# Optimization experiments

Measured on AMD Instinct MI355X. Metric: run time of the kernel, lower is better.

The kernel has to match this reference:

```python
import jax, jax.numpy as jnp
import numpy as np

B, I, H, L, D, O = 2048, 512, 512, 32, 1024, 512
TEMP = 1.0


def _make_params(key):
    ks = jax.random.split(key, 16)
    s = 0.05
    p = {}
    p['in_W'] = jax.random.normal(ks[0], (H, I), jnp.float32) * s
    p['in_b'] = jnp.zeros((H,), jnp.float32)
    p['out_W'] = jax.random.normal(ks[1], (O, H), jnp.float32) * s
    p['out_b'] = jnp.zeros((O,), jnp.float32)
    p['enc_Wih'] = jax.random.normal(ks[2], (4 * H, H), jnp.float32) * s
    p['enc_Whh'] = jax.random.normal(ks[3], (4 * H, H), jnp.float32) * s
    p['enc_bih'] = jnp.zeros((4 * H,), jnp.float32)
    p['enc_bhh'] = jnp.zeros((4 * H,), jnp.float32)
    p['dec_Wih'] = jax.random.normal(ks[4], (4 * H, H), jnp.float32) * s
    p['dec_Whh'] = jax.random.normal(ks[5], (4 * H, H), jnp.float32) * s
    p['dec_bih'] = jnp.zeros((4 * H,), jnp.float32)
    p['dec_bhh'] = jnp.zeros((4 * H,), jnp.float32)
    p['h2t_W'] = jax.random.normal(ks[6], (D, H), jnp.float32) * s
    p['h2t_b'] = jnp.zeros((D,), jnp.float32)
    p['t2h_W'] = jax.random.normal(ks[7], (H, D), jnp.float32) * s
    p['t2h_b'] = jnp.zeros((H,), jnp.float32)
    return p


def setup_inputs() -> dict:
    key = jax.random.key(0)
    k1, k2, k3 = jax.random.split(key, 3)
    inp = {'x': jax.random.normal(k1, (B, I), jnp.float32),
           'gumbel': jax.random.gumbel(k2, (L, B, D), jnp.float32)}
    inp.update(_make_params(k3))
    return inp


def _lstm_cell(x, h, c, Wih, Whh, bih, bhh):
    gates = x @ Wih.T + bih + h @ Whh.T + bhh  # [B, 4H]
    i, f, g, o = jnp.split(gates, 4, axis=-1)
    i = jax.nn.sigmoid(i); f = jax.nn.sigmoid(f)
    g = jnp.tanh(g); o = jax.nn.sigmoid(o)
    c_new = f * c + i * g
    h_new = o * jnp.tanh(c_new)
    return h_new, c_new


def reference(x, gumbel, in_W, in_b, out_W, out_b,
              enc_Wih, enc_Whh, enc_bih, enc_bhh,
              dec_Wih, dec_Whh, dec_bih, dec_bhh,
              h2t_W, h2t_b, t2h_W, t2h_b):
    # ---- encode ----
    x_emb = x @ in_W.T + in_b                      # [B, H]
    hx0 = jnp.zeros((B, H), x.dtype)
    inp0 = jnp.zeros((B, H), x.dtype)

    def enc_step(carry, g_noise):
        hx, cx, inp = carry
        hx, cx = _lstm_cell(inp, hx, cx, enc_Wih, enc_Whh, enc_bih, enc_bhh)
        pre = hx @ h2t_W.T + h2t_b                 # [B, D]
        soft = jax.nn.softmax((pre + g_noise) / TEMP, axis=-1)
        amax = jnp.argmax(soft, axis=-1)           # [B]
        oh = jax.nn.one_hot(amax, D, dtype=soft.dtype)
        z = soft + jax.lax.stop_gradient(oh - soft)  # straight-through
        inp = z @ t2h_W.T + t2h_b
        return (hx, cx, inp), (z, pre, amax)

    # initial cell state is the embedded input (cx = x), per the source
    _, (z_seq, logit_seq, msg_seq) = jax.lax.scan(
        enc_step, (hx0, x_emb, inp0), gumbel)
    one_hot = jnp.transpose(z_seq, (1, 0, 2))      # [B, L, D]
    logits = jnp.transpose(logit_seq, (1, 0, 2))   # [B, L, D]
    messages = msg_seq.T                           # [B, L]

    # ---- decode ----
    z_emb = z_seq @ t2h_W.T + t2h_b                # [L, B, H]

    def dec_step(carry, inp):
        hx, cx = carry
        hx, cx = _lstm_cell(inp, hx, cx, dec_Wih, dec_Whh, dec_bih, dec_bhh)
        return (hx, cx), None

    (hx_final, _), _ = jax.lax.scan(
        dec_step, (jnp.zeros((B, H), x.dtype), jnp.zeros((B, H), x.dtype)), z_emb)
    recon = hx_final @ out_W.T + out_b             # [B, O]
    return recon, one_hot, logits, messages
```

## Files before the change

kernel.cpp:

```cpp
#include <hip/hip_runtime.h>
#include <math.h>

#define B_  2048
#define I_  512
#define H_  512
#define L_  32
#define D_  1024
#define O_  512
#define H4_ 2048
#define KC  32

typedef _Float16 f16x8 __attribute__((ext_vector_type(8)));
typedef _Float16 f16x4 __attribute__((ext_vector_type(4)));
typedef float    f32x4 __attribute__((ext_vector_type(4)));

#define SPLIT_S  1024.0f
#define SPLIT_RS 0.0009765625f

__device__ __forceinline__ void gload16(const _Float16* g, _Float16* l) {
    __builtin_amdgcn_global_load_lds(
        (const __attribute__((address_space(1))) void*)g,
        (__attribute__((address_space(3))) void*)l, 16, 0, 0);
}

__device__ __forceinline__ f16x8 lds_frag(const _Float16* base, int row, int ko) {
    int off = row * 64 + ((((ko >> 3) ^ (row & 7))) << 3);
    return *(const f16x8*)(base + off);
}

__global__ __launch_bounds__(256) void gemm_atb(
    const float* __restrict__ A, const float* __restrict__ W,
    const float* __restrict__ bias, float* __restrict__ C, int ldc,
    float* __restrict__ C2, int ldc2,
    int M, int N, int K)
{
    __shared__ __align__(16) float As[KC][68];
    __shared__ __align__(16) float Ws[KC][68];
    const int tx = threadIdx.x & 15, ty = threadIdx.x >> 4;
    const int m0 = blockIdx.y * 64, n0 = blockIdx.x * 64;
    float acc[4][4] = {};

    for (int k0 = 0; k0 < K; k0 += KC) {
#pragma unroll
        for (int p = 0; p < 2; ++p) {
            int q = threadIdx.x + 256 * p;
            int r = q >> 3, c = q & 7;
            float4 va = *reinterpret_cast<const float4*>(
                &A[(long long)(m0 + r) * K + k0 + c * 4]);
            As[c * 4 + 0][r] = va.x; As[c * 4 + 1][r] = va.y;
            As[c * 4 + 2][r] = va.z; As[c * 4 + 3][r] = va.w;
            float4 vw = *reinterpret_cast<const float4*>(
                &W[(long long)(n0 + r) * K + k0 + c * 4]);
            Ws[c * 4 + 0][r] = vw.x; Ws[c * 4 + 1][r] = vw.y;
            Ws[c * 4 + 2][r] = vw.z; Ws[c * 4 + 3][r] = vw.w;
        }
        __syncthreads();
#pragma unroll
        for (int kk = 0; kk < KC; ++kk) {
            float4 a = *reinterpret_cast<const float4*>(&As[kk][ty * 4]);
            float4 w = *reinterpret_cast<const float4*>(&Ws[kk][tx * 4]);
            float av[4] = {a.x, a.y, a.z, a.w};
            float wv[4] = {w.x, w.y, w.z, w.w};
#pragma unroll
            for (int i = 0; i < 4; ++i)
#pragma unroll
                for (int j = 0; j < 4; ++j)
                    acc[i][j] = fmaf(av[i], wv[j], acc[i][j]);
        }
        __syncthreads();
    }

#pragma unroll
    for (int i = 0; i < 4; ++i) {
        int m = m0 + ty * 4 + i;
        int n = n0 + tx * 4;
        float4 out;
        out.x = acc[i][0]; out.y = acc[i][1]; out.z = acc[i][2]; out.w = acc[i][3];
        if (bias) {
            out.x += bias[n + 0]; out.y += bias[n + 1];
            out.z += bias[n + 2]; out.w += bias[n + 3];
        }
        *reinterpret_cast<float4*>(&C[(long long)m * ldc + n]) = out;
        if (C2)
            *reinterpret_cast<float4*>(&C2[(long long)m * ldc2 + n]) = out;
    }
}

__global__ __launch_bounds__(256) void split_f16(
    const float* __restrict__ src, _Float16* __restrict__ d1,
    _Float16* __restrict__ d2, int n4)
{
    int i = blockIdx.x * 256 + threadIdx.x;
    if (i >= n4) return;
    float4 v = reinterpret_cast<const float4*>(src)[i];
    float vv[4] = {v.x, v.y, v.z, v.w};
    f16x4 o1, o2;
#pragma unroll
    for (int j = 0; j < 4; ++j) {
        _Float16 hh = (_Float16)vv[j];
        o1[j] = hh;
        o2[j] = (_Float16)((vv[j] - (float)hh) * SPLIT_S);
    }
    *reinterpret_cast<f16x4*>(d1 + 4 * i) = o1;
    *reinterpret_cast<f16x4*>(d2 + 4 * i) = o2;
}

__global__ __launch_bounds__(512) void lstm_step_mfma(
    const _Float16* __restrict__ hx1, const _Float16* __restrict__ hx2,
    float* __restrict__ cx,
    const _Float16* __restrict__ W1, const _Float16* __restrict__ W2,
    const float* __restrict__ P,
    const int* __restrict__ m_prev,
    const float* __restrict__ bih, const float* __restrict__ bhh,
    _Float16* __restrict__ ho1, _Float16* __restrict__ ho2,
    float* __restrict__ hof)
{
    __shared__ __align__(16) _Float16 As1[128 * 64];
    __shared__ __align__(16) _Float16 As2[128 * 64];
    __shared__ __align__(16) _Float16 Ws1[128 * 64];
    __shared__ __align__(16) _Float16 Ws2[128 * 64];
    __shared__ int ms[128];

    const int tid = threadIdx.x;
    const int m0 = blockIdx.y * 128, h0 = blockIdx.x * 32;
    const int l = tid & 63, wid = tid >> 6;
    const int wm = wid >> 1, wn = wid & 1;

    if (m_prev != nullptr && tid < 128) ms[tid] = m_prev[m0 + tid];

    f32x4 accM[2][4] = {};
    f32x4 accC[2][4] = {};

    for (int k0 = 0; k0 < H_; k0 += 64) {
#pragma unroll
        for (int s = 0; s < 2; ++s) {
            int seg = wid + s * 8;
            int r   = seg * 8 + (l >> 3);
            int jsw = ((l & 7) ^ (l >> 3)) << 3;
            size_t ga = (size_t)(m0 + r) * H_ + k0 + jsw;
            gload16(hx1 + ga, &As1[seg * 512]);
            gload16(hx2 + ga, &As2[seg * 512]);
            int wrow = ((r >> 4) & 3) * H_ + h0 + ((r >> 6) << 4) + (r & 15);
            size_t gw = (size_t)wrow * H_ + k0 + jsw;
            gload16(W1 + gw, &Ws1[seg * 512]);
            gload16(W2 + gw, &Ws2[seg * 512]);
        }
        __syncthreads();
        const int ac = (l >> 4) << 3;
        const int arow = wm * 32 + (l & 15);
        const int brow = wn * 64 + (l & 15);
#pragma unroll
        for (int kc = 0; kc < 2; ++kc) {
            int ko = kc * 32 + ac;
            f16x8 b1[4], b2[4];
#pragma unroll
            for (int fn = 0; fn < 4; ++fn) {
                b1[fn] = lds_frag(Ws1, brow + fn * 16, ko);
                b2[fn] = lds_frag(Ws2, brow + fn * 16, ko);
            }
#pragma unroll
            for (int fm = 0; fm < 2; ++fm) {
                f16x8 a1 = lds_frag(As1, arow + fm * 16, ko);
                f16x8 a2 = lds_frag(As2, arow + fm * 16, ko);
#pragma unroll
                for (int fn = 0; fn < 4; ++fn) {
                    accM[fm][fn] = __builtin_amdgcn_mfma_f32_16x16x32_f16(
                        a1, b1[fn], accM[fm][fn], 0, 0, 0);
                    accC[fm][fn] = __builtin_amdgcn_mfma_f32_16x16x32_f16(
                        a1, b2[fn], accC[fm][fn], 0, 0, 0);
                    accC[fm][fn] = __builtin_amdgcn_mfma_f32_16x16x32_f16(
                        a2, b1[fn], accC[fm][fn], 0, 0, 0);
                }
            }
        }
        __syncthreads();
    }

    const int hl = l & 15;
    const int h  = h0 + wn * 16 + hl;
    const int rb = m0 + wm * 32 + ((l >> 4) << 2);
    float bs0 = bih[0 * H_ + h] + bhh[0 * H_ + h];
    float bs1 = bih[1 * H_ + h] + bhh[1 * H_ + h];
    float bs2 = bih[2 * H_ + h] + bhh[2 * H_ + h];
    float bs3 = bih[3 * H_ + h] + bhh[3 * H_ + h];
#pragma unroll
    for (int fm = 0; fm < 2; ++fm) {
#pragma unroll
        for (int rg = 0; rg < 4; ++rg) {
            int b = rb + fm * 16 + rg;
            float g0 = accM[fm][0][rg] + SPLIT_RS * accC[fm][0][rg] + bs0;
            float g1 = accM[fm][1][rg] + SPLIT_RS * accC[fm][1][rg] + bs1;
            float g2 = accM[fm][2][rg] + SPLIT_RS * accC[fm][2][rg] + bs2;
            float g3 = accM[fm][3][rg] + SPLIT_RS * accC[fm][3][rg] + bs3;
            if (m_prev != nullptr) {
                const float* Pr = P + (size_t)ms[b - m0] * H4_;
                g0 += Pr[0 * H_ + h]; g1 += Pr[1 * H_ + h];
                g2 += Pr[2 * H_ + h]; g3 += Pr[3 * H_ + h];
            }
            float ig = 1.f / (1.f + expf(-g0));
            float fg = 1.f / (1.f + expf(-g1));
            float gg = tanhf(g2);
            float og = 1.f / (1.f + expf(-g3));
            size_t off = (size_t)b * H_ + h;
            float cnew = fg * cx[off] + ig * gg;
            cx[off] = cnew;
            float hv = og * tanhf(cnew);
            _Float16 hh1 = (_Float16)hv;
            ho1[off] = hh1;
            ho2[off] = (_Float16)((hv - (float)hh1) * SPLIT_S);
            if (hof != nullptr) hof[off] = hv;
        }
    }
}

__global__ __launch_bounds__(256) void gemm_pre_fused(
    const _Float16* __restrict__ A1, const _Float16* __restrict__ A2,
    const _Float16* __restrict__ W1, const _Float16* __restrict__ W2,
    const float* __restrict__ bias,
    float* __restrict__ C2, int ldc2,
    const float* __restrict__ gum,
    float* __restrict__ pbest, int* __restrict__ pidx)
{
    __shared__ __align__(16) _Float16 As1[64 * 64];
    __shared__ __align__(16) _Float16 As2[64 * 64];
    __shared__ __align__(16) _Float16 Ws1[128 * 64];
    __shared__ __align__(16) _Float16 Ws2[128 * 64];
    __shared__ float cb[2][64];
    __shared__ int   ci[2][64];

    const int tid = threadIdx.x;
    const int m0 = blockIdx.y * 64, n0 = blockIdx.x * 128;
    const int l = tid & 63, wid = tid >> 6;
    const int wm = wid >> 1, wn = wid & 1;

    f32x4 accM[2][4] = {};
    f32x4 accC[2][4] = {};

    for (int k0 = 0; k0 < H_; k0 += 64) {
#pragma unroll
        for (int s = 0; s < 2; ++s) {
            int seg = wid + s * 4;
            int r   = seg * 8 + (l >> 3);
            int jsw = ((l & 7) ^ (l >> 3)) << 3;
            size_t ga = (size_t)(m0 + r) * H_ + k0 + jsw;
            gload16(A1 + ga, &As1[seg * 512]);
            gload16(A2 + ga, &As2[seg * 512]);
        }
#pragma unroll
        for (int s = 0; s < 4; ++s) {
            int seg = wid + s * 4;
            int r   = seg * 8 + (l >> 3);
            int jsw = ((l & 7) ^ (l >> 3)) << 3;
            size_t gw = (size_t)(n0 + r) * H_ + k0 + jsw;
            gload16(W1 + gw, &Ws1[seg * 512]);
            gload16(W2 + gw, &Ws2[seg * 512]);
        }
        __syncthreads();
        const int ac = (l >> 4) << 3;
        const int arow = wm * 32 + (l & 15);
        const int brow = wn * 64 + (l & 15);
#pragma unroll
        for (int kc = 0; kc < 2; ++kc) {
            int ko = kc * 32 + ac;
            f16x8 b1[4], b2[4];
#pragma unroll
            for (int fn = 0; fn < 4; ++fn) {
                b1[fn] = lds_frag(Ws1, brow + fn * 16, ko);
                b2[fn] = lds_frag(Ws2, brow + fn * 16, ko);
            }
#pragma unroll
            for (int fm = 0; fm < 2; ++fm) {
                f16x8 a1 = lds_frag(As1, arow + fm * 16, ko);
                f16x8 a2 = lds_frag(As2, arow + fm * 16, ko);
#pragma unroll
                for (int fn = 0; fn < 4; ++fn) {
                    accM[fm][fn] = __builtin_amdgcn_mfma_f32_16x16x32_f16(
                        a1, b1[fn], accM[fm][fn], 0, 0, 0);
                    accC[fm][fn] = __builtin_amdgcn_mfma_f32_16x16x32_f16(
                        a1, b2[fn], accC[fm][fn], 0, 0, 0);
                    accC[fm][fn] = __builtin_amdgcn_mfma_f32_16x16x32_f16(
                        a2, b1[fn], accC[fm][fn], 0, 0, 0);
                }
            }
        }
        __syncthreads();
    }

    const int hl = l & 15;
    const int g4 = l >> 4;
    const int rb = m0 + wm * 32 + (g4 << 2);
    float vbest[2][4]; int vidx[2][4];
#pragma unroll
    for (int fm = 0; fm < 2; ++fm)
#pragma unroll
        for (int rg = 0; rg < 4; ++rg) { vbest[fm][rg] = -INFINITY; vidx[fm][rg] = 0; }

#pragma unroll
    for (int fn = 0; fn < 4; ++fn) {
        int d = n0 + wn * 64 + fn * 16 + hl;
        float bv = bias[d];
#pragma unroll
        for (int fm = 0; fm < 2; ++fm)
#pragma unroll
            for (int rg = 0; rg < 4; ++rg) {
                int b = rb + fm * 16 + rg;
                float v = accM[fm][fn][rg] + SPLIT_RS * accC[fm][fn][rg] + bv;
                C2[(size_t)b * ldc2 + d] = v;
                float t = v + gum[(size_t)b * D_ + d];
                if (t > vbest[fm][rg]) { vbest[fm][rg] = t; vidx[fm][rg] = d; }
            }
    }

#pragma unroll
    for (int off = 1; off < 16; off <<= 1) {
#pragma unroll
        for (int fm = 0; fm < 2; ++fm)
#pragma unroll
            for (int rg = 0; rg < 4; ++rg) {
                float ov = __shfl_xor(vbest[fm][rg], off);
                int   oi = __shfl_xor(vidx[fm][rg], off);
                if (ov > vbest[fm][rg] ||
                    (ov == vbest[fm][rg] && oi < vidx[fm][rg])) {
                    vbest[fm][rg] = ov; vidx[fm][rg] = oi;
                }
            }
    }
    if (hl == 0) {
#pragma unroll
        for (int fm = 0; fm < 2; ++fm)
#pragma unroll
            for (int rg = 0; rg < 4; ++rg) {
                int rl = wm * 32 + fm * 16 + (g4 << 2) + rg;
                cb[wn][rl] = vbest[fm][rg];
                ci[wn][rl] = vidx[fm][rg];
            }
    }
    __syncthreads();
    if (tid < 64) {
        float b0 = cb[0][tid]; int i0 = ci[0][tid];
        float b1v = cb[1][tid]; int i1 = ci[1][tid];
        if (b1v > b0 || (b1v == b0 && i1 < i0)) { b0 = b1v; i0 = i1; }
        pbest[(size_t)(m0 + tid) * 8 + blockIdx.x] = b0;
        pidx [(size_t)(m0 + tid) * 8 + blockIdx.x] = i0;
    }
}

__global__ __launch_bounds__(256) void argmax_fin(
    const float* __restrict__ pbest, const int* __restrict__ pidx,
    float* __restrict__ onehot, float* __restrict__ messages,
    int* __restrict__ m_out, int l)
{
    int b = blockIdx.x * 256 + threadIdx.x;
    float best = -INFINITY; int bi = 0;
#pragma unroll
    for (int j = 0; j < 8; ++j) {
        float v = pbest[(size_t)b * 8 + j];
        int   i = pidx [(size_t)b * 8 + j];
        if (v > best || (v == best && i < bi)) { best = v; bi = i; }
    }
    m_out[b] = bi;
    messages[(size_t)b * L_ + l] = (float)bi;
    onehot[((size_t)b * L_ + l) * D_ + bi] = 1.0f;
}

__global__ __launch_bounds__(256) void build_emb(
    const float* __restrict__ t2h_W, const float* __restrict__ t2h_b,
    float* __restrict__ emb)
{
    int idx = blockIdx.x * 256 + threadIdx.x;
    int d = idx >> 9, h = idx & (H_ - 1);
    emb[idx] = t2h_W[(long long)h * D_ + d] + t2h_b[h];
}

extern "C" void kernel_launch(void* const* d_in, const int* in_sizes, int n_in,
                              void* d_out, int out_size, void* d_ws, size_t ws_size,
                              hipStream_t stream)
{
    (void)in_sizes; (void)n_in; (void)out_size; (void)ws_size;
    const float* x       = (const float*)d_in[0];
    const float* gumbel  = (const float*)d_in[1];
    const float* in_W    = (const float*)d_in[2];
    const float* in_b    = (const float*)d_in[3];
    const float* out_W   = (const float*)d_in[4];
    const float* out_b   = (const float*)d_in[5];
    const float* enc_Wih = (const float*)d_in[6];
    const float* enc_Whh = (const float*)d_in[7];
    const float* enc_bih = (const float*)d_in[8];
    const float* enc_bhh = (const float*)d_in[9];
    const float* dec_Wih = (const float*)d_in[10];
    const float* dec_Whh = (const float*)d_in[11];
    const float* dec_bih = (const float*)d_in[12];
    const float* dec_bhh = (const float*)d_in[13];
    const float* h2t_W   = (const float*)d_in[14];
    const float* h2t_b   = (const float*)d_in[15];
    const float* t2h_W   = (const float*)d_in[16];
    const float* t2h_b   = (const float*)d_in[17];

    float* out      = (float*)d_out;
    float* recon    = out;
    float* onehot   = out + (size_t)B_ * O_;
    float* logits   = onehot + (size_t)B_ * L_ * D_;
    float* messages = logits + (size_t)B_ * L_ * D_;

    float* ws    = (float*)d_ws;
    float* cx    = ws;
    float* emb   = cx + (size_t)B_ * H_;
    float* P_enc = emb + (size_t)D_ * H_;
    float* P_dec = P_enc + (size_t)D_ * H4_;
    float* hxf   = P_dec + (size_t)D_ * H4_;
    float* pbest = hxf + (size_t)B_ * H_;
    int*   pidx  = (int*)(pbest + (size_t)B_ * 8);
    int*   m_all = pidx + (size_t)B_ * 8;
    _Float16* fb   = (_Float16*)(m_all + (size_t)L_ * B_);
    _Float16* hxA1 = fb;  fb += (size_t)B_ * H_;
    _Float16* hxA2 = fb;  fb += (size_t)B_ * H_;
    _Float16* hxB1 = fb;  fb += (size_t)B_ * H_;
    _Float16* hxB2 = fb;  fb += (size_t)B_ * H_;
    _Float16* encW1 = fb; fb += (size_t)H4_ * H_;
    _Float16* encW2 = fb; fb += (size_t)H4_ * H_;
    _Float16* decW1 = fb; fb += (size_t)H4_ * H_;
    _Float16* decW2 = fb; fb += (size_t)H4_ * H_;
    _Float16* h2t1  = fb; fb += (size_t)D_ * H_;
    _Float16* h2t2  = fb;

    const dim3 blk256(256);

    hipMemsetAsync(hxA1, 0, (size_t)B_ * H_ * 4, stream);
    hipMemsetAsync(onehot, 0, (size_t)B_ * L_ * D_ * sizeof(float), stream);

    split_f16<<<dim3((H4_ * H_ / 4) / 256), blk256, 0, stream>>>(
        enc_Whh, encW1, encW2, H4_ * H_ / 4);
    split_f16<<<dim3((H4_ * H_ / 4) / 256), blk256, 0, stream>>>(
        dec_Whh, decW1, decW2, H4_ * H_ / 4);
    split_f16<<<dim3((D_ * H_ / 4) / 256), blk256, 0, stream>>>(
        h2t_W, h2t1, h2t2, D_ * H_ / 4);

    gemm_atb<<<dim3(H_ / 64, B_ / 64), blk256, 0, stream>>>(
        x, in_W, in_b, cx, H_, nullptr, 0, B_, H_, I_);

    build_emb<<<dim3((D_ * H_) / 256), blk256, 0, stream>>>(t2h_W, t2h_b, emb);
    gemm_atb<<<dim3(H4_ / 64, D_ / 64), blk256, 0, stream>>>(
        emb, enc_Wih, nullptr, P_enc, H4_, nullptr, 0, D_, H4_, H_);
    gemm_atb<<<dim3(H4_ / 64, D_ / 64), blk256, 0, stream>>>(
        emb, dec_Wih, nullptr, P_dec, H4_, nullptr, 0, D_, H4_, H_);

    _Float16 *c1 = hxA1, *c2 = hxA2, *n1 = hxB1, *n2 = hxB2;
    for (int l = 0; l < L_; ++l) {
        lstm_step_mfma<<<dim3(H_ / 32, B_ / 128), dim3(512), 0, stream>>>(
            c1, c2, cx, encW1, encW2, P_enc,
            (l == 0) ? nullptr : (m_all + (size_t)(l - 1) * B_),
            enc_bih, enc_bhh, n1, n2, nullptr);
        { _Float16* t = c1; c1 = n1; n1 = t; t = c2; c2 = n2; n2 = t; }
        gemm_pre_fused<<<dim3(D_ / 128, B_ / 64), blk256, 0, stream>>>(
            c1, c2, h2t1, h2t2, h2t_b,
            logits + (size_t)l * D_, L_ * D_,
            gumbel + (size_t)l * B_ * D_, pbest, pidx);
        argmax_fin<<<dim3(B_ / 256), blk256, 0, stream>>>(
            pbest, pidx, onehot, messages, m_all + (size_t)l * B_, l);
    }

    hipMemsetAsync(c1, 0, (size_t)B_ * H_ * 2, stream);
    hipMemsetAsync(c2, 0, (size_t)B_ * H_ * 2, stream);
    hipMemsetAsync(cx, 0, (size_t)B_ * H_ * sizeof(float), stream);
    for (int l = 0; l < L_; ++l) {
        lstm_step_mfma<<<dim3(H_ / 32, B_ / 128), dim3(512), 0, stream>>>(
            c1, c2, cx, decW1, decW2, P_dec, m_all + (size_t)l * B_,
            dec_bih, dec_bhh, n1, n2, (l == L_ - 1) ? hxf : nullptr);
        { _Float16* t = c1; c1 = n1; n1 = t; t = c2; c2 = n2; n2 = t; }
    }

    gemm_atb<<<dim3(O_ / 64, B_ / 64), blk256, 0, stream>>>(
        hxf, out_W, out_b, recon, O_, nullptr, 0, B_, O_, H_);
}
```

Before: 3.169 ms.

## Double-buffer LDS tiles in LSTM and logits GEMMs and fuse argmax finalize

Both the LSTM step kernel and the fused logits GEMM now keep two LDS buffers, so the async global-to-LDS loads for the next K tile are issued while MFMAs run on the current one. The separate argmax_fin launch per encoder step is removed. Instead the last block to finish each row group, found with an atomic counter and threadfences, reduces the partial maxima and writes the message and one-hot entry. This doubles LDS use, which may lower occupancy, and adds atomic/fence overhead in exchange for fewer launches and overlapped loads.

Result: slower. 3.555 ms (+12.2%).

```diff
diff --git a/kernel.cpp b/kernel.cpp
--- a/kernel.cpp
+++ b/kernel.cpp
@@ -115,15 +115,15 @@
     _Float16* __restrict__ ho1, _Float16* __restrict__ ho2,
     float* __restrict__ hof)
 {
-    __shared__ __align__(16) _Float16 As1[128 * 64];
-    __shared__ __align__(16) _Float16 As2[128 * 64];
-    __shared__ __align__(16) _Float16 Ws1[128 * 64];
-    __shared__ __align__(16) _Float16 Ws2[128 * 64];
+    __shared__ __align__(16) _Float16 As1[2][128 * 64];
+    __shared__ __align__(16) _Float16 As2[2][128 * 64];
+    __shared__ __align__(16) _Float16 Ws1[2][128 * 64];
+    __shared__ __align__(16) _Float16 Ws2[2][128 * 64];
     __shared__ int ms[128];
 
     const int tid = threadIdx.x;
     const int m0 = blockIdx.y * 128, h0 = blockIdx.x * 32;
-    const int l = tid & 63, wid = tid >> 6;
+    const int ln = tid & 63, wid = tid >> 6;
     const int wm = wid >> 1, wn = wid & 1;
 
     if (m_prev != nullptr && tid < 128) ms[tid] = m_prev[m0 + tid];
@@ -131,37 +131,49 @@
     f32x4 accM[2][4] = {};
     f32x4 accC[2][4] = {};
 
-    for (int k0 = 0; k0 < H_; k0 += 64) {
+    auto stage = [&](int buf, int k0) {
 #pragma unroll
         for (int s = 0; s < 2; ++s) {
             int seg = wid + s * 8;
-            int r   = seg * 8 + (l >> 3);
-            int jsw = ((l & 7) ^ (l >> 3)) << 3;
+            int r   = seg * 8 + (ln >> 3);
+            int jsw = ((ln & 7) ^ (ln >> 3)) << 3;
             size_t ga = (size_t)(m0 + r) * H_ + k0 + jsw;
-            gload16(hx1 + ga, &As1[seg * 512]);
-            gload16(hx2 + ga, &As2[seg * 512]);
+            gload16(hx1 + ga, &As1[buf][seg * 512]);
+            gload16(hx2 + ga, &As2[buf][seg * 512]);
             int wrow = ((r >> 4) & 3) * H_ + h0 + ((r >> 6) << 4) + (r & 15);
             size_t gw = (size_t)wrow * H_ + k0 + jsw;
-            gload16(W1 + gw, &Ws1[seg * 512]);
-            gload16(W2 + gw, &Ws2[seg * 512]);
-        }
-        __syncthreads();
-        const int ac = (l >> 4) << 3;
-        const int arow = wm * 32 + (l & 15);
-        const int brow = wn * 64 + (l & 15);
+            gload16(W1 + gw, &Ws1[buf][seg * 512]);
+            gload16(W2 + gw, &Ws2[buf][seg * 512]);
+        }
+    };
+
+    stage(0, 0);
+    __syncthreads();
+
+    const int ac = (ln >> 4) << 3;
+    const int arow = wm * 32 + (ln & 15);
+    const int brow = wn * 64 + (ln & 15);
+    int cur = 0;
+
+    for (int t = 0; t < 8; ++t) {
+        if (t < 7) stage(cur ^ 1, (t + 1) * 64);
+        const _Float16* a1b = &As1[cur][0];
+        const _Float16* a2b = &As2[cur][0];
+        const _Float16* w1b = &Ws1[cur][0];
+        const _Float16* w2b = &Ws2[cur][0];
 #pragma unroll
         for (int kc = 0; kc < 2; ++kc) {
             int ko = kc * 32 + ac;
             f16x8 b1[4], b2[4];
 #pragma unroll
             for (int fn = 0; fn < 4; ++fn) {
-                b1[fn] = lds_frag(Ws1, brow + fn * 16, ko);
-                b2[fn] = lds_frag(Ws2, brow + fn * 16, ko);
+                b1[fn] = lds_frag(w1b, brow + fn * 16, ko);
+                b2[fn] = lds_frag(w2b, brow + fn * 16, ko);
             }
 #pragma unroll
             for (int fm = 0; fm < 2; ++fm) {
-                f16x8 a1 = lds_frag(As1, arow + fm * 16, ko);
-                f16x8 a2 = lds_frag(As2, arow + fm * 16, ko);
+                f16x8 a1 = lds_frag(a1b, arow + fm * 16, ko);
+                f16x8 a2 = lds_frag(a2b, arow + fm * 16, ko);
 #pragma unroll
                 for (int fn = 0; fn < 4; ++fn) {
                     accM[fm][fn] = __builtin_amdgcn_mfma_f32_16x16x32_f16(
@@ -174,11 +186,12 @@
             }
         }
         __syncthreads();
-    }
-
-    const int hl = l & 15;
+        cur ^= 1;
+    }
+
+    const int hl = ln & 15;
     const int h  = h0 + wn * 16 + hl;
-    const int rb = m0 + wm * 32 + ((l >> 4) << 2);
+    const int rb = m0 + wm * 32 + ((ln >> 4) << 2);
     float bs0 = bih[0 * H_ + h] + bhh[0 * H_ + h];
     float bs1 = bih[1 * H_ + h] + bhh[1 * H_ + h];
     float bs2 = bih[2 * H_ + h] + bhh[2 * H_ + h];
@@ -219,59 +232,75 @@
     const float* __restrict__ bias,
     float* __restrict__ C2, int ldc2,
     const float* __restrict__ gum,
-    float* __restrict__ pbest, int* __restrict__ pidx)
+    float* __restrict__ pbest, int* __restrict__ pidx,
+    int* __restrict__ cnt,
+    float* __restrict__ onehot, float* __restrict__ messages,
+    int* __restrict__ m_out, int l)
 {
-    __shared__ __align__(16) _Float16 As1[64 * 64];
-    __shared__ __align__(16) _Float16 As2[64 * 64];
-    __shared__ __align__(16) _Float16 Ws1[128 * 64];
-    __shared__ __align__(16) _Float16 Ws2[128 * 64];
+    __shared__ __align__(16) _Float16 As1[2][64 * 64];
+    __shared__ __align__(16) _Float16 As2[2][64 * 64];
+    __shared__ __align__(16) _Float16 Ws1[2][128 * 64];
+    __shared__ __align__(16) _Float16 Ws2[2][128 * 64];
     __shared__ float cb[2][64];
     __shared__ int   ci[2][64];
+    __shared__ int   lastf;
 
     const int tid = threadIdx.x;
     const int m0 = blockIdx.y * 64, n0 = blockIdx.x * 128;
-    const int l = tid & 63, wid = tid >> 6;
+    const int ln = tid & 63, wid = tid >> 6;
     const int wm = wid >> 1, wn = wid & 1;
 
     f32x4 accM[2][4] = {};
     f32x4 accC[2][4] = {};
 
-    for (int k0 = 0; k0 < H_; k0 += 64) {
+    auto stage = [&](int buf, int k0) {
 #pragma unroll
         for (int s = 0; s < 2; ++s) {
             int seg = wid + s * 4;
-            int r   = seg * 8 + (l >> 3);
-            int jsw = ((l & 7) ^ (l >> 3)) << 3;
+            int r   = seg * 8 + (ln >> 3);
+            int jsw = ((ln & 7) ^ (ln >> 3)) << 3;
             size_t ga = (size_t)(m0 + r) * H_ + k0 + jsw;
-            gload16(A1 + ga, &As1[seg * 512]);
-            gload16(A2 + ga, &As2[seg * 512]);
+            gload16(A1 + ga, &As1[buf][seg * 512]);
+            gload16(A2 + ga, &As2[buf][seg * 512]);
         }
 #pragma unroll
         for (int s = 0; s < 4; ++s) {
             int seg = wid + s * 4;
-            int r   = seg * 8 + (l >> 3);
-            int jsw = ((l & 7) ^ (l >> 3)) << 3;
+            int r   = seg * 8 + (ln >> 3);
+            int jsw = ((ln & 7) ^ (ln >> 3)) << 3;
             size_t gw = (size_t)(n0 + r) * H_ + k0 + jsw;
-            gload16(W1 + gw, &Ws1[seg * 512]);
-            gload16(W2 + gw, &Ws2[seg * 512]);
-        }
-        __syncthreads();
-        const int ac = (l >> 4) << 3;
-        const int arow = wm * 32 + (l & 15);
-        const int brow = wn * 64 + (l & 15);
+            gload16(W1 + gw, &Ws1[buf][seg * 512]);
+            gload16(W2 + gw, &Ws2[buf][seg * 512]);
+        }
+    };
+
+    stage(0, 0);
+    __syncthreads();
+
+    const int ac = (ln >> 4) << 3;
+    const int arow = wm * 32 + (ln & 15);
+    const int brow = wn * 64 + (ln & 15);
+    int cur = 0;
+
+    for (int t = 0; t < 8; ++t) {
+        if (t < 7) stage(cur ^ 1, (t + 1) * 64);
+        const _Float16* a1b = &As1[cur][0];
+        const _Float16* a2b = &As2[cur][0];
+        const _Float16* w1b = &Ws1[cur][0];
+        const _Float16* w2b = &Ws2[cur][0];
 #pragma unroll
         for (int kc = 0; kc < 2; ++kc) {
             int ko = kc * 32 + ac;
             f16x8 b1[4], b2[4];
 #pragma unroll
             for (int fn = 0; fn < 4; ++fn) {
-                b1[fn] = lds_frag(Ws1, brow + fn * 16, ko);
-                b2[fn] = lds_frag(Ws2, brow + fn * 16, ko);
+                b1[fn] = lds_frag(w1b, brow + fn * 16, ko);
+                b2[fn] = lds_frag(w2b, brow + fn * 16, ko);
             }
 #pragma unroll
             for (int fm = 0; fm < 2; ++fm) {
-                f16x8 a1 = lds_frag(As1, arow + fm * 16, ko);
-                f16x8 a2 = lds_frag(As2, arow + fm * 16, ko);
+                f16x8 a1 = lds_frag(a1b, arow + fm * 16, ko);
+                f16x8 a2 = lds_frag(a2b, arow + fm * 16, ko);
 #pragma unroll
                 for (int fn = 0; fn < 4; ++fn) {
                     accM[fm][fn] = __builtin_amdgcn_mfma_f32_16x16x32_f16(
@@ -284,10 +313,11 @@
             }
         }
         __syncthreads();
-    }
-
-    const int hl = l & 15;
-    const int g4 = l >> 4;
+        cur ^= 1;
+    }
+
+    const int hl = ln & 15;
+    const int g4 = ln >> 4;
     const int rb = m0 + wm * 32 + (g4 << 2);
     float vbest[2][4]; int vidx[2][4];
 #pragma unroll
@@ -342,25 +372,29 @@
         if (b1v > b0 || (b1v == b0 && i1 < i0)) { b0 = b1v; i0 = i1; }
         pbest[(size_t)(m0 + tid) * 8 + blockIdx.x] = b0;
         pidx [(size_t)(m0 + tid) * 8 + blockIdx.x] = i0;
-    }
-}
-
-__global__ __launch_bounds__(256) void argmax_fin(
-    const float* __restrict__ pbest, const int* __restrict__ pidx,
-    float* __restrict__ onehot, float* __restrict__ messages,
-    int* __restrict__ m_out, int l)
-{
-    int b = blockIdx.x * 256 + threadIdx.x;
-    float best = -INFINITY; int bi = 0;
-#pragma unroll
-    for (int j = 0; j < 8; ++j) {
-        float v = pbest[(size_t)b * 8 + j];
-        int   i = pidx [(size_t)b * 8 + j];
-        if (v > best || (v == best && i < bi)) { best = v; bi = i; }
-    }
-    m_out[b] = bi;
-    messages[(size_t)b * L_ + l] = (float)bi;
-    onehot[((size_t)b * L_ + l) * D_ + bi] = 1.0f;
+        __threadfence();
+    }
+    __syncthreads();
+    if (tid == 0)
+        lastf = (atomicAdd(cnt + blockIdx.y, 1) == 7);
+    __syncthreads();
+    if (lastf) {
+        __threadfence();
+        if (tid < 64) {
+            int b = m0 + tid;
+            volatile const float* pb = pbest + (size_t)b * 8;
+            volatile const int*   pi = pidx  + (size_t)b * 8;
+            float best = -INFINITY; int bi = 0;
+#pragma unroll
+            for (int j = 0; j < 8; ++j) {
+                float v = pb[j]; int i = pi[j];
+                if (v > best || (v == best && i < bi)) { best = v; bi = i; }
+            }
+            m_out[b] = bi;
+            messages[(size_t)b * L_ + l] = (float)bi;
+            onehot[((size_t)b * L_ + l) * D_ + bi] = 1.0f;
+        }
+    }
 }
 
 __global__ __launch_bounds__(256) void build_emb(
@@ -411,7 +445,8 @@
     float* pbest = hxf + (size_t)B_ * H_;
     int*   pidx  = (int*)(pbest + (size_t)B_ * 8);
     int*   m_all = pidx + (size_t)B_ * 8;
-    _Float16* fb   = (_Float16*)(m_all + (size_t)L_ * B_);
+    int*   cnt   = m_all + (size_t)L_ * B_;
+    _Float16* fb   = (_Float16*)(cnt + L_ * 32);
     _Float16* hxA1 = fb;  fb += (size_t)B_ * H_;
     _Float16* hxA2 = fb;  fb += (size_t)B_ * H_;
     _Float16* hxB1 = fb;  fb += (size_t)B_ * H_;
@@ -425,8 +460,9 @@
 
     const dim3 blk256(256);
 
-    hipMemsetAsync(hxA1, 0, (size_t)B_ * H_ * 4, stream);
-    hipMemsetAsync(onehot, 0, (size_t)B_ * L_ * D_ * sizeof(float), stream);
+    (void)hipMemsetAsync(hxA1, 0, (size_t)B_ * H_ * 4, stream);
+    (void)hipMemsetAsync(onehot, 0, (size_t)B_ * L_ * D_ * sizeof(float), stream);
+    (void)hipMemsetAsync(cnt, 0, (size_t)L_ * 32 * sizeof(int), stream);
 
     split_f16<<<dim3((H4_ * H_ / 4) / 256), blk256, 0, stream>>>(
         enc_Whh, encW1, encW2, H4_ * H_ / 4);
@@ -454,14 +490,13 @@
         gemm_pre_fused<<<dim3(D_ / 128, B_ / 64), blk256, 0, stream>>>(
             c1, c2, h2t1, h2t2, h2t_b,
             logits + (size_t)l * D_, L_ * D_,
-            gumbel + (size_t)l * B_ * D_, pbest, pidx);
-        argmax_fin<<<dim3(B_ / 256), blk256, 0, stream>>>(
-            pbest, pidx, onehot, messages, m_all + (size_t)l * B_, l);
-    }
-
-    hipMemsetAsync(c1, 0, (size_t)B_ * H_ * 2, stream);
-    hipMemsetAsync(c2, 0, (size_t)B_ * H_ * 2, stream);
-    hipMemsetAsync(cx, 0, (size_t)B_ * H_ * sizeof(float), stream);
+            gumbel + (size_t)l * B_ * D_, pbest, pidx,
+            cnt + l * 32, onehot, messages, m_all + (size_t)l * B_, l);
+    }
+
+    (void)hipMemsetAsync(c1, 0, (size_t)B_ * H_ * 2, stream);
+    (void)hipMemsetAsync(c2, 0, (size_t)B_ * H_ * 2, stream);
+    (void)hipMemsetAsync(cx, 0, (size_t)B_ * H_ * sizeof(float), stream);
     for (int l = 0; l < L_; ++l) {
         lstm_step_mfma<<<dim3(H_ / 32, B_ / 128), dim3(512), 0, stream>>>(
             c1, c2, cx, decW1, decW2, P_dec, m_all + (size_t)l * B_,
```
